# Performance work log

Measured on AMD Instinct MI355X. Metric: run time of the kernel, lower is better.

Reference implementation:

```python
import jax, jax.numpy as jnp
import numpy as np

B, N, DIM = 1, 1024, 512
H, DH = 8, 64
TOPK_RATIO = 0.1
SCALE = DH ** -0.5
PH = 32  # phase MLP hidden = hidden_dim//2 = 64//2
INIT_SCALE = 0.02


def cayley(Mre, Mim):
    # CayleyLinear: unitary weight W = (I - A)^{-1} (I + A), A skew-Hermitian
    M = (Mre + 1j * Mim).astype(jnp.complex64) * INIT_SCALE
    A = M - M.conj().T
    I = jnp.eye(M.shape[0], dtype=M.dtype)
    return jnp.linalg.solve(I - A, I + A)


def phase_fn(mag, pw1, pb1, pw2, pb2):
    # PhaseModulation: MLP(|alpha|) + 0.1*|alpha| residual
    h = jax.nn.silu(mag[..., None] @ pw1 + pb1)  # (...,PH)
    out = (h @ pw2 + pb2)[..., 0]
    return out + mag * 0.1


def setup_inputs() -> dict:
    key = jax.random.key(0)
    ks = jax.random.split(key, 12)
    d = {
        'x_real': jax.random.normal(ks[0], (B, N, DIM), dtype=jnp.float32),
        'x_imag': jax.random.normal(ks[1], (B, N, DIM), dtype=jnp.float32),
    }
    for i, n in enumerate(['Wq', 'Wk', 'Wv', 'Wo']):
        d[n + '_re'] = jax.random.normal(ks[2 + 2 * i], (DIM, DIM), dtype=jnp.float32)
        d[n + '_im'] = jax.random.normal(ks[3 + 2 * i], (DIM, DIM), dtype=jnp.float32)
    d['pw1'] = jax.random.normal(ks[10], (1, PH), dtype=jnp.float32) * 0.1
    d['pb1'] = jnp.zeros((PH,), dtype=jnp.float32)
    d['pw2'] = jax.random.normal(ks[11], (PH, 1), dtype=jnp.float32) * 0.1
    d['pb2'] = jnp.zeros((1,), dtype=jnp.float32)
    return d


def reference(x_real, x_imag, Wq_re, Wq_im, Wk_re, Wk_im, Wv_re, Wv_im,
              Wo_re, Wo_im, pw1, pb1, pw2, pb2):
    x = (x_real + 1j * x_imag).astype(jnp.complex64)  # (B,N,D)
    Q = x @ cayley(Wq_re, Wq_im)
    K = x @ cayley(Wk_re, Wk_im)
    V = x @ cayley(Wv_re, Wv_im)
    # (B,N,D) -> (B,H,N,DH)
    Q = Q.reshape(B, N, H, DH).transpose(0, 2, 1, 3)
    K = K.reshape(B, N, H, DH).transpose(0, 2, 1, 3)
    V = V.reshape(B, N, H, DH).transpose(0, 2, 1, 3)
    # complex inner products: conj(Q) . K
    alpha = jnp.einsum('bhnd,bhsd->bhns', Q.conj(), K) * SCALE  # (B,H,N,N) complex
    mag = jnp.abs(alpha)
    phase = phase_fn(jax.lax.stop_gradient(mag), pw1, pb1, pw2, pb2)
    beta = alpha * jnp.exp(1j * phase.astype(jnp.complex64))
    # Born-rule normalization: p = |beta|^2 / sum |beta|^2
    b2 = beta.real ** 2 + beta.imag ** 2
    probs = b2 / b2.sum(axis=-1, keepdims=True)  # (B,H,N,N) real
    # top-k interference routing
    k = max(1, int(TOPK_RATIO * N))
    tp, ti = jax.lax.top_k(probs, k)  # (B,H,N,k)
    tpn = tp / (tp.sum(axis=-1, keepdims=True) + 1e-8)
    w = jax.nn.softmax(tpn * k, axis=-1)  # complex_softmax on real input
    # gather V rows per (b,h): (N,DH)[(N,k)] -> (N,k,DH), no NxN expand
    gather = jax.vmap(jax.vmap(lambda v, i: v[i]))
    V_topk = gather(V, ti)  # (B,H,N,k,DH) complex
    out = (w[..., None] * V_topk).sum(axis=3)  # (B,H,N,DH)
    out = out.transpose(0, 2, 1, 3).reshape(B, N, DIM)
    out = out @ cayley(Wo_re, Wo_im)
    return out  # complex64 (B,N,DIM)
```

## Files before the change

kernel.cpp:

```cpp
#include <hip/hip_runtime.h>
#include <math.h>


#define PLANE   262144
#define CMAT    524288
#define PPLANE  524288
#define CPROJ   1048576
#define KTOP    102

#define R_FLOATS 12582912
#define POOL_FLOATS (4*CMAT + 8192 + R_FLOATS)
__device__ __attribute__((aligned(256))) float g_pool[POOL_FLOATS];

__launch_bounds__(256)
__global__ void cgemm_kernel(
    const float* __restrict__ Are, const float* __restrict__ Aim, int sA,
    const float* __restrict__ Bre, const float* __restrict__ Bim, int sB,
    const float* __restrict__ Dre, const float* __restrict__ Dim, int sD,
    const float* __restrict__ Ere2, float* __restrict__ Ewr, int sE,
    float* __restrict__ Cre, float* __restrict__ Cim, int sC,
    int M, int N, int Kd, float dcoef, int mode, int out_floats)
{
    __shared__ float As_re[2][32][34], As_im[2][32][34];
    __shared__ float Bs_re[2][32][68], Bs_im[2][32][68];
    const int b = blockIdx.z;
    Are += (size_t)b * sA; Aim += (size_t)b * sA;
    Bre += (size_t)b * sB; Bim += (size_t)b * sB;
    Dre += (size_t)b * sD; Dim += (size_t)b * sD;
    const float* Ere = Ere2 + (size_t)b * sE;
    const float* Eim = Ere + PLANE;
    float* Uwr = Ewr ? (Ewr + (size_t)b * sE) : (float*)0;
    Cre += (size_t)b * sC; Cim += (size_t)b * sC;
    const int bnd = mode == 5 ? (out_floats - b * sC) : 0;
    const int tid = threadIdx.x;
    const int bm = blockIdx.y * 32, bn = blockIdx.x * 64;
    const int tm = (tid >> 4) << 1;
    const int tn = (tid & 15) << 2;
    const int lmA = tid >> 3;
    const int lkA = (tid & 7) << 2;
    const int lkB = tid >> 4;
    const int lnB = (tid & 15) << 2;
    float cr[2][4] = {{0.f}}, ci[2][4] = {{0.f}};
    const float* pAre = Are + (size_t)(bm + lmA) * Kd + lkA;
    const float* pAim = Aim + (size_t)(bm + lmA) * Kd + lkA;
    const float* pBre = Bre + (size_t)lkB * N + bn + lnB;
    const float* pBim = Bim + (size_t)lkB * N + bn + lnB;
    float4 ar  = *(const float4*)(pAre);
    float4 ai  = *(const float4*)(pAim);
    float4 br0 = *(const float4*)(pBre);
    float4 bi0 = *(const float4*)(pBim);
    float4 br1 = *(const float4*)(pBre + (size_t)16 * N);
    float4 bi1 = *(const float4*)(pBim + (size_t)16 * N);
    for (int k0 = 0; k0 < Kd; k0 += 32) {
        const int buf = (k0 >> 5) & 1;
        As_re[buf][lkA+0][lmA] = ar.x; As_re[buf][lkA+1][lmA] = ar.y;
        As_re[buf][lkA+2][lmA] = ar.z; As_re[buf][lkA+3][lmA] = ar.w;
        As_im[buf][lkA+0][lmA] = ai.x; As_im[buf][lkA+1][lmA] = ai.y;
        As_im[buf][lkA+2][lmA] = ai.z; As_im[buf][lkA+3][lmA] = ai.w;
        *(float4*)&Bs_re[buf][lkB][lnB] = br0;
        *(float4*)&Bs_im[buf][lkB][lnB] = bi0;
        *(float4*)&Bs_re[buf][lkB+16][lnB] = br1;
        *(float4*)&Bs_im[buf][lkB+16][lnB] = bi1;
        __syncthreads();
        const int kn = k0 + 32;
        if (kn < Kd) {
            ar  = *(const float4*)(pAre + kn);
            ai  = *(const float4*)(pAim + kn);
            br0 = *(const float4*)(pBre + (size_t)kn * N);
            bi0 = *(const float4*)(pBim + (size_t)kn * N);
            br1 = *(const float4*)(pBre + (size_t)(kn + 16) * N);
            bi1 = *(const float4*)(pBim + (size_t)(kn + 16) * N);
        }
        #pragma unroll
        for (int k = 0; k < 32; ++k) {
            const float2 xr = *(const float2*)&As_re[buf][k][tm];
            const float2 xi = *(const float2*)&As_im[buf][k][tm];
            const float4 yr = *(const float4*)&Bs_re[buf][k][tn];
            const float4 yi = *(const float4*)&Bs_im[buf][k][tn];
            const float axr[2] = {xr.x, xr.y};
            const float axi[2] = {xi.x, xi.y};
            const float byr[4] = {yr.x, yr.y, yr.z, yr.w};
            const float byi[4] = {yi.x, yi.y, yi.z, yi.w};
            #pragma unroll
            for (int i = 0; i < 2; ++i) {
                #pragma unroll
                for (int j = 0; j < 4; ++j) {
                    cr[i][j] += axr[i]*byr[j] - axi[i]*byi[j];
                    ci[i][j] += axr[i]*byi[j] + axi[i]*byr[j];
                }
            }
        }
    }
    #pragma unroll
    for (int i = 0; i < 2; ++i) {
        const int row = bm + tm + i;
        const size_t idx = (size_t)row * N + bn + tn;
        float vr[4] = {cr[i][0], cr[i][1], cr[i][2], cr[i][3]};
        float vi[4] = {ci[i][0], ci[i][1], ci[i][2], ci[i][3]};
        if (mode == 1) {
            const float4 dr4 = *(const float4*)(Dre + idx);
            const float4 di4 = *(const float4*)(Dim + idx);
            const float dr[4] = {dr4.x, dr4.y, dr4.z, dr4.w};
            const float di[4] = {di4.x, di4.y, di4.z, di4.w};
            #pragma unroll
            for (int j = 0; j < 4; ++j) { vr[j] = dcoef*dr[j] - vr[j]; vi[j] = dcoef*di[j] - vi[j]; }
        } else if (mode == 2) {
            const float4 dr4 = *(const float4*)(Dre + idx);
            const float4 di4 = *(const float4*)(Dim + idx);
            const float dr[4] = {dr4.x, dr4.y, dr4.z, dr4.w};
            const float di[4] = {di4.x, di4.y, di4.z, di4.w};
            float ur[4], ui[4];
            #pragma unroll
            for (int j = 0; j < 4; ++j) { ur[j] = 5.5f*dr[j] + 0.5f*vr[j]; ui[j] = 5.5f*di[j] + 0.5f*vi[j]; }
            *(float4*)(Uwr + idx) = make_float4(ur[0], ur[1], ur[2], ur[3]);
            *(float4*)(Uwr + PLANE + idx) = make_float4(ui[0], ui[1], ui[2], ui[3]);
        } else if (mode == 3) {
            const float inv61 = 1.0f/61.5f;
            const float4 sr4 = *(const float4*)(Dre + idx);
            const float4 si4 = *(const float4*)(Dim + idx);
            const float4 s2r = *(const float4*)(Ere + idx);
            const float4 s2i = *(const float4*)(Eim + idx);
            const float sr[4] = {sr4.x, sr4.y, sr4.z, sr4.w};
            const float si[4] = {si4.x, si4.y, si4.z, si4.w};
            const float tr[4] = {s2r.x, s2r.y, s2r.z, s2r.w};
            const float ti[4] = {s2i.x, s2i.y, s2i.z, s2i.w};
            #pragma unroll
            for (int j = 0; j < 4; ++j) {
                const float diag = (row == bn + tn + j) ? 60.5f : 0.0f;
                vr[j] = (diag + 48.f*sr[j] + 23.f*tr[j] + vr[j]) * inv61;
                vi[j] = (       48.f*si[j] + 23.f*ti[j] + vi[j]) * inv61;
            }
        } else if (mode == 4) {
            const float4 dr4 = *(const float4*)(Dre + idx);
            const float4 di4 = *(const float4*)(Dim + idx);
            const float dr[4] = {dr4.x, dr4.y, dr4.z, dr4.w};
            const float di[4] = {di4.x, di4.y, di4.z, di4.w};
            #pragma unroll
            for (int j = 0; j < 4; ++j) {
                const float diag = (row == bn + tn + j) ? 1.0f : 0.0f;
                vr[j] = 2.f*dr[j] + 2.f*vr[j] - diag;
                vi[j] = 2.f*di[j] + 2.f*vi[j];
            }
        }
        if (mode == 5) {
            #pragma unroll
            for (int j = 0; j < 4; ++j) {
                const size_t ire = idx + j;
                const size_t iim = (size_t)PPLANE + idx + j;
                if (ire < (size_t)bnd) Cre[ire] = vr[j];
                if (iim < (size_t)bnd) Cre[iim] = vi[j];
            }
        } else {
            *(float4*)(Cre + idx) = make_float4(vr[0], vr[1], vr[2], vr[3]);
            *(float4*)(Cim + idx) = make_float4(vi[0], vi[1], vi[2], vi[3]);
        }
    }
}

__launch_bounds__(256)
__global__ void build_A_kernel(const float* __restrict__ W0re, const float* __restrict__ W0im,
                               const float* __restrict__ W1re, const float* __restrict__ W1im,
                               const float* __restrict__ W2re, const float* __restrict__ W2im,
                               const float* __restrict__ W3re, const float* __restrict__ W3im,
                               int aoff)
{
    float* Aout = g_pool + aoff;
    const int w = blockIdx.y;
    const float* Mre; const float* Mim;
    if      (w == 0) { Mre = W0re; Mim = W0im; }
    else if (w == 1) { Mre = W1re; Mim = W1im; }
    else if (w == 2) { Mre = W2re; Mim = W2im; }
    else             { Mre = W3re; Mim = W3im; }
    const int idx = blockIdx.x * 256 + threadIdx.x;
    const int i = idx >> 9, j = idx & 511;
    float* Are = Aout + (size_t)w * CMAT;
    float* Aim = Are + PLANE;
    Are[idx] = 0.02f * (Mre[i*512 + j] - Mre[j*512 + i]);
    Aim[idx] = 0.02f * (Mim[i*512 + j] + Mim[j*512 + i]);
}

__launch_bounds__(256)
__global__ void zero_kernel(float* __restrict__ p, int n)
{
    const int i = blockIdx.x * 256 + threadIdx.x;
    if (i < n) p[i] = 0.f;
}

__launch_bounds__(256)
__global__ void scores_kernel(const float* __restrict__ Qre, const float* __restrict__ Qim,
                              const float* __restrict__ Kre, const float* __restrict__ Kim,
                              float* __restrict__ B2, float* __restrict__ RS)
{
    __shared__ float Qs_re[64][68], Qs_im[64][68], Ks_re[64][68], Ks_im[64][68];
    __shared__ float rs[64];
    const int h = blockIdx.z;
    const int bm = blockIdx.y * 64, bn = blockIdx.x * 64;
    const int tid = threadIdx.x;
    const int tm = (tid >> 4) << 2, tn = (tid & 15) << 2;
    const int lm = tid >> 2;
    const int lk = (tid & 3) << 4;
    #pragma unroll
    for (int q = 0; q < 4; ++q) {
        const int kb = lk + 4*q;
        const float4 qr = *(const float4*)(Qre + (size_t)(bm+lm)*512 + h*64 + kb);
        const float4 qi = *(const float4*)(Qim + (size_t)(bm+lm)*512 + h*64 + kb);
        const float4 kr = *(const float4*)(Kre + (size_t)(bn+lm)*512 + h*64 + kb);
        const float4 ki = *(const float4*)(Kim + (size_t)(bn+lm)*512 + h*64 + kb);
        Qs_re[kb+0][lm]=qr.x; Qs_re[kb+1][lm]=qr.y; Qs_re[kb+2][lm]=qr.z; Qs_re[kb+3][lm]=qr.w;
        Qs_im[kb+0][lm]=qi.x; Qs_im[kb+1][lm]=qi.y; Qs_im[kb+2][lm]=qi.z; Qs_im[kb+3][lm]=qi.w;
        Ks_re[kb+0][lm]=kr.x; Ks_re[kb+1][lm]=kr.y; Ks_re[kb+2][lm]=kr.z; Ks_re[kb+3][lm]=kr.w;
        Ks_im[kb+0][lm]=ki.x; Ks_im[kb+1][lm]=ki.y; Ks_im[kb+2][lm]=ki.z; Ks_im[kb+3][lm]=ki.w;
    }
    if (tid < 64) rs[tid] = 0.f;
    __syncthreads();
    float dr[4][4] = {{0.f}}, di[4][4] = {{0.f}};
    #pragma unroll
    for (int k = 0; k < 64; ++k) {
        const float4 xr = *(const float4*)&Qs_re[k][tm];
        const float4 xi = *(const float4*)&Qs_im[k][tm];
        const float4 yr = *(const float4*)&Ks_re[k][tn];
        const float4 yi = *(const float4*)&Ks_im[k][tn];
        const float axr[4] = {xr.x, xr.y, xr.z, xr.w};
        const float axi[4] = {xi.x, xi.y, xi.z, xi.w};
        const float byr[4] = {yr.x, yr.y, yr.z, yr.w};
        const float byi[4] = {yi.x, yi.y, yi.z, yi.w};
        #pragma unroll
        for (int i = 0; i < 4; ++i) {
            #pragma unroll
            for (int j = 0; j < 4; ++j) {
                dr[i][j] += axr[i]*byr[j] + axi[i]*byi[j];
                di[i][j] += axr[i]*byi[j] - axi[i]*byr[j];
            }
        }
    }
    float rpart[4] = {0.f, 0.f, 0.f, 0.f};
    #pragma unroll
    for (int i = 0; i < 4; ++i) {
        #pragma unroll
        for (int j = 0; j < 4; ++j) {
            const float b2v = (dr[i][j]*dr[i][j] + di[i][j]*di[i][j]) * 0.015625f;
            B2[(size_t)h*1048576 + (size_t)(bm+tm+i)*1024 + (bn+tn+j)] = b2v;
            rpart[i] += b2v;
        }
    }
    #pragma unroll
    for (int i = 0; i < 4; ++i) atomicAdd(&rs[tm+i], rpart[i]);
    __syncthreads();
    if (tid < 64) atomicAdd(&RS[h*1024 + bm + tid], rs[tid]);
}

__launch_bounds__(256)
__global__ void select_kernel(const float* __restrict__ B2, const float* __restrict__ RS,
                              const float* __restrict__ Vre, const float* __restrict__ Vim,
                              float* __restrict__ AOre, float* __restrict__ AOim)
{
    __shared__ float sv[1024];
    __shared__ unsigned int hist[256];
    __shared__ int ssum[256];
    __shared__ unsigned int sc[4];
    __shared__ float sel_v[104];
    __shared__ int sel_i[104];
    __shared__ float sel_w[104];
    __shared__ float rbuf[256];
    const int bid = blockIdx.x;
    const int h = bid >> 10, n = bid & 1023;
    const int tid = threadIdx.x;
    const float* row = B2 + (size_t)h * 1048576 + (size_t)n * 1024;
    #pragma unroll
    for (int e = 0; e < 4; ++e) sv[tid + 256*e] = row[tid + 256*e];
    if (tid == 0) sc[2] = 0u;
    __syncthreads();

    unsigned prefix = 0u, pmask = 0u;
    int krem = KTOP;
    for (int pass = 0; pass < 4; ++pass) {
        const int shift = 24 - 8 * pass;
        hist[tid] = 0u;
        __syncthreads();
        #pragma unroll
        for (int e = 0; e < 4; ++e) {
            const unsigned u = __float_as_uint(sv[tid + 256*e]);
            if ((u & pmask) == prefix) atomicAdd(&hist[(u >> shift) & 255u], 1u);
        }
        __syncthreads();
        ssum[tid] = (int)hist[tid];
        __syncthreads();
        for (int off = 1; off < 256; off <<= 1) {
            const int add = (tid + off < 256) ? ssum[tid + off] : 0;
            __syncthreads();
            ssum[tid] += add;
            __syncthreads();
        }
        const int above = (tid < 255) ? ssum[tid + 1] : 0;
        if (ssum[tid] >= krem && above < krem) {
            sc[0] = (unsigned)tid;
            sc[1] = (unsigned)(krem - above);
        }
        __syncthreads();
        prefix |= sc[0] << shift;
        pmask |= 0xFFu << shift;
        krem = (int)sc[1];
        __syncthreads();
    }
    const unsigned T = prefix;
    const int m = krem;

    #pragma unroll
    for (int e = 0; e < 4; ++e) {
        const int i = tid + 256*e;
        const float v = sv[i];
        const unsigned u = __float_as_uint(v);
        bool sel = (u > T);
        if (!sel && u == T) {
            int rank = 0;
            for (int j = 0; j < i; ++j) rank += (__float_as_uint(sv[j]) == T) ? 1 : 0;
            sel = (rank < m);
        }
        if (sel) {
            const unsigned p = atomicAdd(&sc[2], 1u);
            if (p < 104u) { sel_v[p] = v; sel_i[p] = i; }
        }
    }
    __syncthreads();

    rbuf[tid] = (tid < KTOP) ? sel_v[tid] : 0.f;
    __syncthreads();
    for (int st = 128; st > 0; st >>= 1) { if (tid < st) rbuf[tid] += rbuf[tid + st]; __syncthreads(); }
    const float sumtop = rbuf[0];
    __syncthreads();
    rbuf[tid] = (tid < KTOP) ? sel_v[tid] : -1.f;
    __syncthreads();
    for (int st = 128; st > 0; st >>= 1) { if (tid < st) rbuf[tid] = fmaxf(rbuf[tid], rbuf[tid + st]); __syncthreads(); }
    const float vmax = rbuf[0];
    __syncthreads();

    const float S_row = RS[(h << 10) + n];
    const float denom = sumtop + 1e-8f * S_row;
    const float scl = (float)KTOP / denom;
    if (tid < KTOP) sel_w[tid] = expf(sel_v[tid] * scl - vmax * scl);
    __syncthreads();
    rbuf[tid] = (tid < KTOP) ? sel_w[tid] : 0.f;
    __syncthreads();
    for (int st = 128; st > 0; st >>= 1) { if (tid < st) rbuf[tid] += rbuf[tid + st]; __syncthreads(); }
    const float Z = rbuf[0];
    __syncthreads();

    if (tid < 128) {
        const int d = tid & 63;
        const int im = tid >> 6;
        const float* Vp = im ? Vim : Vre;
        const int base = h * 64 + d;
        float acc = 0.f;
        for (int j = 0; j < KTOP; ++j) acc += sel_w[j] * Vp[(size_t)sel_i[j] * 512 + base];
        acc /= Z;
        float* AOp = im ? AOim : AOre;
        AOp[(size_t)n * 512 + h * 64 + d] = acc;
    }
}

extern "C" void kernel_launch(void* const* d_in, const int* in_sizes, int n_in,
                              void* d_out, int out_size, void* d_ws, size_t ws_size,
                              hipStream_t stream)
{
    (void)in_sizes; (void)n_in; (void)d_ws; (void)ws_size;
    const float* x_re = (const float*)d_in[0];
    const float* x_im = (const float*)d_in[1];

    float* pool = nullptr;
    hipGetSymbolAddress((void**)&pool, HIP_SYMBOL(g_pool));

    float* Wall = pool;
    float* RSg  = Wall + 4*CMAT;
    float* R    = RSg + 8192;
    float* A  = R;
    float* S  = R + 4*CMAT;
    float* S2 = R + 8*CMAT;
    float* X  = R + 12*CMAT;
    float* X2 = R + 16*CMAT;
    float* T  = R + 20*CMAT;
    float* Q  = R;
    float* Kp = R + CPROJ;
    float* V  = R + 2*CPROJ;
    float* AO = R + 3*CPROJ;
    float* B2 = R + 4*CPROJ;

    const int aoff = (int)(A - pool);

    build_A_kernel<<<dim3(1024,4),256,0,stream>>>(
        (const float*)d_in[2],(const float*)d_in[3],(const float*)d_in[4],(const float*)d_in[5],
        (const float*)d_in[6],(const float*)d_in[7],(const float*)d_in[8],(const float*)d_in[9], aoff);
    cgemm_kernel<<<dim3(8,16,4),256,0,stream>>>(A,A+PLANE,CMAT, A,A+PLANE,CMAT,
                                                A,A+PLANE,CMAT, A,nullptr,CMAT,
                                                S,S+PLANE,CMAT, 512,512,512, 0.f, 0, 0);
    cgemm_kernel<<<dim3(8,16,4),256,0,stream>>>(S,S+PLANE,CMAT, S,S+PLANE,CMAT,
                                                S,S+PLANE,CMAT, S,X,CMAT,
                                                S2,S2+PLANE,CMAT, 512,512,512, 0.f, 2, 0);
    cgemm_kernel<<<dim3(8,16,4),256,0,stream>>>(S2,S2+PLANE,CMAT, X,X+PLANE,CMAT,
                                                S,S+PLANE,CMAT, S2,nullptr,CMAT,
                                                X2,X2+PLANE,CMAT, 512,512,512, 0.f, 3, 0);
    float* Xc = X2; float* Xn = X;
    for (int it = 0; it < 2; ++it) {
        cgemm_kernel<<<dim3(8,16,4),256,0,stream>>>(S,S+PLANE,CMAT, Xc,Xc+PLANE,CMAT,
                                                    Xc,Xc+PLANE,CMAT, S,nullptr,CMAT,
                                                    T,T+PLANE,CMAT, 512,512,512, 1.f, 1, 0);
        cgemm_kernel<<<dim3(8,16,4),256,0,stream>>>(Xc,Xc+PLANE,CMAT, T,T+PLANE,CMAT,
                                                    Xc,Xc+PLANE,CMAT, S,nullptr,CMAT,
                                                    Xn,Xn+PLANE,CMAT, 512,512,512, 2.f, 1, 0);
        float* tmp = Xc; Xc = Xn; Xn = tmp;
    }
    cgemm_kernel<<<dim3(8,16,4),256,0,stream>>>(A,A+PLANE,CMAT, Xc,Xc+PLANE,CMAT,
                                                Xc,Xc+PLANE,CMAT, S,nullptr,CMAT,
                                                Wall,Wall+PLANE,CMAT, 512,512,512, 0.f, 4, 0);

    cgemm_kernel<<<dim3(8,32,3),256,0,stream>>>(x_re,x_im,0, Wall,Wall+PLANE,CMAT,
                                                x_re,x_im,0, S,nullptr,0,
                                                Q,Q+PPLANE,CPROJ, 1024,512,512, 0.f, 0, 0);

    zero_kernel<<<32,256,0,stream>>>(RSg, 8192);
    scores_kernel<<<dim3(16,16,8),256,0,stream>>>(Q,Q+PPLANE, Kp,Kp+PPLANE, B2, RSg);
    select_kernel<<<8192,256,0,stream>>>(B2, RSg, V,V+PPLANE, AO,AO+PPLANE);

    cgemm_kernel<<<dim3(8,16,2),256,0,stream>>>(AO,AO+PPLANE,PLANE, Wall+3*CMAT,Wall+3*CMAT+PLANE,0,
                                                AO,AO+PPLANE,0, S,nullptr,0,
                                                (float*)d_out,nullptr,PLANE, 512,512,512, 0.f, 5, out_size);
}
```

Measured before the change: 1.019 ms.

## Compute row sums in select, use wave-shuffle prefix scan, tile build_A transpose

Drops the atomic row-sum accumulation in the scores kernel and the zero kernel; each select block now reduces its own row in shared memory. The 256-entry histogram suffix scan switches from a log-step shared-memory scan with many barriers to wavefront shuffles plus a 4-wave combine. build_A now transposes through a shared-memory tile so its reads are coalesced. The aim is fewer launches, atomics and barriers, at the cost of an extra reduction per select block.

```diff
diff --git a/kernel.cpp b/kernel.cpp
--- a/kernel.cpp
+++ b/kernel.cpp
@@ -164,35 +164,41 @@
                                const float* __restrict__ W3re, const float* __restrict__ W3im,
                                int aoff)
 {
+    __shared__ float Tre[32][33], Tim[32][33];
     float* Aout = g_pool + aoff;
-    const int w = blockIdx.y;
+    const int w = blockIdx.z;
     const float* Mre; const float* Mim;
     if      (w == 0) { Mre = W0re; Mim = W0im; }
     else if (w == 1) { Mre = W1re; Mim = W1im; }
     else if (w == 2) { Mre = W2re; Mim = W2im; }
     else             { Mre = W3re; Mim = W3im; }
-    const int idx = blockIdx.x * 256 + threadIdx.x;
-    const int i = idx >> 9, j = idx & 511;
     float* Are = Aout + (size_t)w * CMAT;
     float* Aim = Are + PLANE;
-    Are[idx] = 0.02f * (Mre[i*512 + j] - Mre[j*512 + i]);
-    Aim[idx] = 0.02f * (Mim[i*512 + j] + Mim[j*512 + i]);
-}
-
-__launch_bounds__(256)
-__global__ void zero_kernel(float* __restrict__ p, int n)
-{
-    const int i = blockIdx.x * 256 + threadIdx.x;
-    if (i < n) p[i] = 0.f;
+    const int r = blockIdx.y * 32, c = blockIdx.x * 32;
+    const int tx = threadIdx.x & 31, ty = threadIdx.x >> 5;
+    #pragma unroll
+    for (int p = 0; p < 4; ++p) {
+        const int rr = ty + 8*p;
+        Tre[rr][tx] = Mre[(size_t)(c+rr)*512 + r + tx];
+        Tim[rr][tx] = Mim[(size_t)(c+rr)*512 + r + tx];
+    }
+    __syncthreads();
+    #pragma unroll
+    for (int p = 0; p < 4; ++p) {
+        const int rr = ty + 8*p;
+        const int i = r + rr, j = c + tx;
+        const size_t o = (size_t)i*512 + j;
+        Are[o] = 0.02f * (Mre[o] - Tre[tx][rr]);
+        Aim[o] = 0.02f * (Mim[o] + Tim[tx][rr]);
+    }
 }
 
 __launch_bounds__(256)
 __global__ void scores_kernel(const float* __restrict__ Qre, const float* __restrict__ Qim,
                               const float* __restrict__ Kre, const float* __restrict__ Kim,
-                              float* __restrict__ B2, float* __restrict__ RS)
+                              float* __restrict__ B2)
 {
     __shared__ float Qs_re[64][68], Qs_im[64][68], Ks_re[64][68], Ks_im[64][68];
-    __shared__ float rs[64];
     const int h = blockIdx.z;
     const int bm = blockIdx.y * 64, bn = blockIdx.x * 64;
     const int tid = threadIdx.x;
@@ -211,7 +217,6 @@
         Ks_re[kb+0][lm]=kr.x; Ks_re[kb+1][lm]=kr.y; Ks_re[kb+2][lm]=kr.z; Ks_re[kb+3][lm]=kr.w;
         Ks_im[kb+0][lm]=ki.x; Ks_im[kb+1][lm]=ki.y; Ks_im[kb+2][lm]=ki.z; Ks_im[kb+3][lm]=ki.w;
     }
-    if (tid < 64) rs[tid] = 0.f;
     __syncthreads();
     float dr[4][4] = {{0.f}}, di[4][4] = {{0.f}};
     #pragma unroll
@@ -233,35 +238,31 @@
             }
         }
     }
-    float rpart[4] = {0.f, 0.f, 0.f, 0.f};
     #pragma unroll
     for (int i = 0; i < 4; ++i) {
         #pragma unroll
         for (int j = 0; j < 4; ++j) {
             const float b2v = (dr[i][j]*dr[i][j] + di[i][j]*di[i][j]) * 0.015625f;
             B2[(size_t)h*1048576 + (size_t)(bm+tm+i)*1024 + (bn+tn+j)] = b2v;
-            rpart[i] += b2v;
-        }
-    }
-    #pragma unroll
-    for (int i = 0; i < 4; ++i) atomicAdd(&rs[tm+i], rpart[i]);
-    __syncthreads();
-    if (tid < 64) atomicAdd(&RS[h*1024 + bm + tid], rs[tid]);
+        }
+    }
 }
 
 __launch_bounds__(256)
-__global__ void select_kernel(const float* __restrict__ B2, const float* __restrict__ RS,
+__global__ void select_kernel(const float* __restrict__ B2,
                               const float* __restrict__ Vre, const float* __restrict__ Vim,
                               float* __restrict__ AOre, float* __restrict__ AOim)
 {
     __shared__ float sv[1024];
     __shared__ unsigned int hist[256];
     __shared__ int ssum[256];
+    __shared__ int wtot[4];
     __shared__ unsigned int sc[4];
     __shared__ float sel_v[104];
     __shared__ int sel_i[104];
     __shared__ float sel_w[104];
     __shared__ float rbuf[256];
+    __shared__ float srow_sh;
     const int bid = blockIdx.x;
     const int h = bid >> 10, n = bid & 1023;
     const int tid = threadIdx.x;
@@ -271,6 +272,13 @@
     if (tid == 0) sc[2] = 0u;
     __syncthreads();
 
+    rbuf[tid] = sv[tid] + sv[tid+256] + sv[tid+512] + sv[tid+768];
+    __syncthreads();
+    for (int st = 128; st > 0; st >>= 1) { if (tid < st) rbuf[tid] += rbuf[tid + st]; __syncthreads(); }
+    if (tid == 0) srow_sh = rbuf[0];
+    __syncthreads();
+
+    const int lane = tid & 63, wv = tid >> 6;
     unsigned prefix = 0u, pmask = 0u;
     int krem = KTOP;
     for (int pass = 0; pass < 4; ++pass) {
@@ -283,14 +291,18 @@
             if ((u & pmask) == prefix) atomicAdd(&hist[(u >> shift) & 255u], 1u);
         }
         __syncthreads();
-        ssum[tid] = (int)hist[tid];
-        __syncthreads();
-        for (int off = 1; off < 256; off <<= 1) {
-            const int add = (tid + off < 256) ? ssum[tid + off] : 0;
-            __syncthreads();
-            ssum[tid] += add;
-            __syncthreads();
-        }
+        int v = (int)hist[tid];
+        #pragma unroll
+        for (int off = 1; off < 64; off <<= 1) {
+            const int o = __shfl_down(v, off);
+            if (lane + off < 64) v += o;
+        }
+        if (lane == 0) wtot[wv] = v;
+        __syncthreads();
+        int addv = 0;
+        for (int w2 = wv + 1; w2 < 4; ++w2) addv += wtot[w2];
+        ssum[tid] = v + addv;
+        __syncthreads();
         const int above = (tid < 255) ? ssum[tid + 1] : 0;
         if (ssum[tid] >= krem && above < krem) {
             sc[0] = (unsigned)tid;
@@ -334,8 +346,7 @@
     const float vmax = rbuf[0];
     __syncthreads();
 
-    const float S_row = RS[(h << 10) + n];
-    const float denom = sumtop + 1e-8f * S_row;
+    const float denom = sumtop + 1e-8f * srow_sh;
     const float scl = (float)KTOP / denom;
     if (tid < KTOP) sel_w[tid] = expf(sel_v[tid] * scl - vmax * scl);
     __syncthreads();
@@ -370,8 +381,7 @@
     hipGetSymbolAddress((void**)&pool, HIP_SYMBOL(g_pool));
 
     float* Wall = pool;
-    float* RSg  = Wall + 4*CMAT;
-    float* R    = RSg + 8192;
+    float* R    = Wall + 4*CMAT + 8192;
     float* A  = R;
     float* S  = R + 4*CMAT;
     float* S2 = R + 8*CMAT;
@@ -386,7 +396,7 @@
 
     const int aoff = (int)(A - pool);
 
-    build_A_kernel<<<dim3(1024,4),256,0,stream>>>(
+    build_A_kernel<<<dim3(16,16,4),256,0,stream>>>(
         (const float*)d_in[2],(const float*)d_in[3],(const float*)d_in[4],(const float*)d_in[5],
         (const float*)d_in[6],(const float*)d_in[7],(const float*)d_in[8],(const float*)d_in[9], aoff);
     cgemm_kernel<<<dim3(8,16,4),256,0,stream>>>(A,A+PLANE,CMAT, A,A+PLANE,CMAT,
@@ -416,9 +426,8 @@
                                                 x_re,x_im,0, S,nullptr,0,
                                                 Q,Q+PPLANE,CPROJ, 1024,512,512, 0.f, 0, 0);
 
-    zero_kernel<<<32,256,0,stream>>>(RSg, 8192);
-    scores_kernel<<<dim3(16,16,8),256,0,stream>>>(Q,Q+PPLANE, Kp,Kp+PPLANE, B2, RSg);
-    select_kernel<<<8192,256,0,stream>>>(B2, RSg, V,V+PPLANE, AO,AO+PPLANE);
+    scores_kernel<<<dim3(16,16,8),256,0,stream>>>(Q,Q+PPLANE, Kp,Kp+PPLANE, B2);
+    select_kernel<<<8192,256,0,stream>>>(B2, V,V+PPLANE, AO,AO+PPLANE);
 
     cgemm_kernel<<<dim3(8,16,2),256,0,stream>>>(AO,AO+PPLANE,PLANE, Wall+3*CMAT,Wall+3*CMAT+PLANE,0,
                                                 AO,AO+PPLANE,0, S,nullptr,0,
```

Result: no change. 1.003 ms (median of 2 runs) (-1.6%).
